# Optimization experiments

Hardware: AMD Instinct MI355X
Metric: run time of the kernel (lower is better)

Reference implementation:

```python
import jax, jax.numpy as jnp
import numpy as np

B, S, D, E, N = 2, 1024, 1024, 64, 16  # batch, seq, model_dim, embedding_dim, num_splats


def setup_inputs() -> dict:
    key = jax.random.key(0)
    ks = jax.random.split(key, 8)
    inv_sqrt_d = 1.0 / np.sqrt(D)
    return {
        "token_embeddings": jax.random.normal(ks[0], (B, S, D), jnp.float32),
        # position encoder Linear(D, E)
        "pos_W": jax.random.normal(ks[1], (D, E), jnp.float32) * inv_sqrt_d,
        "pos_b": jnp.zeros((E,), jnp.float32),
        "positional_bias": jax.random.normal(ks[2], (1024, E), jnp.float32) * 0.01,
        "splat_positions": jax.random.normal(ks[3], (N, E), jnp.float32) * 0.2,
        "splat_log_scales": jnp.zeros((N,), jnp.float32),
        # q/k/v Linear(D, D, bias=False)
        "q_W": jax.random.normal(ks[4], (D, D), jnp.float32) * inv_sqrt_d,
        "k_W": jax.random.normal(ks[5], (D, D), jnp.float32) * inv_sqrt_d,
        "v_W": jax.random.normal(ks[6], (D, D), jnp.float32) * inv_sqrt_d,
        "splat_gates": jnp.full((N,), 0.5, jnp.float32),
        "residual_weight": jnp.asarray(0.8, jnp.float32),
        "ln_w": jnp.ones((D,), jnp.float32),
        "ln_b": jnp.zeros((D,), jnp.float32),
    }


def reference(token_embeddings, pos_W, pos_b, positional_bias, splat_positions,
              splat_log_scales, q_W, k_W, v_W, splat_gates, residual_weight,
              ln_w, ln_b):
    b, s, d = token_embeddings.shape
    # token positions in splat embedding space: tanh(Linear(x)) + pos_bias[:S]
    positions = jnp.tanh(token_embeddings @ pos_W + pos_b) + positional_bias[:s][None]  # [B,S,E]
    # spatial influence per splat: Gaussian of distance, clamped scales, floor 0.01
    diff = positions[:, :, None, :] - splat_positions[None, None]  # [B,S,N,E]
    dist_sq = jnp.sum(diff * diff, axis=-1)                         # [B,S,N]
    scales = jnp.clip(jnp.exp(splat_log_scales), 0.3, 2.0)
    influence = jnp.maximum(jnp.exp(-0.5 * dist_sq / (scales * scales)), 0.01)  # [B,S,N]

    q = token_embeddings @ q_W
    k = token_embeddings @ k_W
    v = token_embeddings @ v_W

    w = jnp.transpose(influence, (2, 0, 1))      # [N,B,S]
    qw = q[None] * w[..., None]                  # [N,B,S,D]
    kw = k[None] * w[..., None]
    scores = jnp.einsum('nbid,nbjd->nbij', qw, kw) / jnp.sqrt(jnp.asarray(d, jnp.float32))
    causal = jnp.tril(jnp.ones((s, s), bool))
    scores = jnp.where(causal[None, None], scores, -1e9)
    attn = jax.nn.softmax(scores, axis=-1)       # [N,B,S,S]
    out = jnp.einsum('nbij,bjd->nbid', attn, v)  # [N,B,S,D]

    gates = jax.nn.sigmoid(splat_gates)[:, None, None, None]
    combined = jnp.mean(out * gates, axis=0)     # [B,S,D]

    rw = jax.nn.sigmoid(residual_weight)
    o = rw * token_embeddings + (1.0 - rw) * combined
    # LayerNorm (eps=1e-5)
    mu = jnp.mean(o, axis=-1, keepdims=True)
    var = jnp.mean((o - mu) ** 2, axis=-1, keepdims=True)
    return (o - mu) / jnp.sqrt(var + 1e-5) * ln_w + ln_b
```

## Files before the change

kernel.cpp:

```cpp
#include <hip/hip_runtime.h>
#include <hip/hip_bf16.h>
#include <hip/hip_fp16.h>

using bf16 = __hip_bfloat16;
typedef __attribute__((ext_vector_type(8))) short short8;
typedef __attribute__((ext_vector_type(4))) float f32x4;

static constexpr int Bb = 2, Ss = 1024, Dd = 1024, Ee = 64, Nn = 16;

struct Params {
    const float *X, *posW, *posB, *pbias, *spos, *lsc, *qW, *kW, *vW, *gates, *rwp, *lnw, *lnb;
    bf16 *Xb, *Wt, *WpT, *QKV, *Vt, *Aav;
    __half *wh;
    float *qk[4], *cb[4], *out;
};

__device__ __forceinline__ unsigned short f2bfr(float f) {
    __hip_bfloat16 h = __float2bfloat16(f);
    return *reinterpret_cast<unsigned short*>(&h);
}

#define GL_LDS(gp, lp) __builtin_amdgcn_global_load_lds( \
    (const __attribute__((address_space(1))) void*)(gp), \
    (__attribute__((address_space(3))) void*)(lp), 16, 0, 0)

__device__ __forceinline__ void do_transpose_f2b(
    const float* __restrict__ in, bf16* __restrict__ out,
    int R, int C, int bx, int by, char* sm)
{
    float (*tile)[65] = (float(*)[65])sm;
    int tx = threadIdx.x & 63, ty = threadIdx.x >> 6;
    int r0 = by * 64, c0 = bx * 64;
    #pragma unroll
    for (int i = 0; i < 16; ++i)
        tile[ty + i*4][tx] = in[(long)(r0 + ty + i*4)*C + c0 + tx];
    __syncthreads();
    #pragma unroll
    for (int i = 0; i < 16; ++i)
        out[(long)(c0 + ty + i*4)*R + r0 + tx] = __float2bfloat16(tile[tx][ty + i*4]);
    __syncthreads();
}

__device__ __forceinline__ void do_gemm64(
    const bf16* __restrict__ Ab, const bf16* __restrict__ Bw, float* __restrict__ C,
    int Nc, int m0, int n0, int kBeg, int kEnd, float scale, char* sm)
{
    int tid = threadIdx.x, wid = tid >> 6, lane = tid & 63;
    int wn = wid * 32, r16 = lane & 15, quad = lane >> 4;

    f32x4 acc[4][2];
    #pragma unroll
    for (int i = 0; i < 4; ++i)
        #pragma unroll
        for (int j = 0; j < 2; ++j)
            #pragma unroll
            for (int c = 0; c < 4; ++c) acc[i][j][c] = 0.f;

    const short* Ag = (const short*)Ab;
    const short* Bg = (const short*)Bw;

    int arow[2], akg[2], brow[4], bkg[4];
    #pragma unroll
    for (int j = 0; j < 2; ++j) {
        int c = tid + j*256; arow[j] = c >> 3; akg[j] = (c & 7) ^ (arow[j] & 7);
    }
    #pragma unroll
    for (int j = 0; j < 4; ++j) {
        int c = tid + j*256; brow[j] = c >> 3; bkg[j] = (c & 7) ^ (brow[j] & 7);
    }

    auto stage = [&](int k0, int cr) {
        short* sA = (short*)(sm + cr*24576);
        short* sB = (short*)(sm + cr*24576 + 8192);
        #pragma unroll
        for (int j = 0; j < 2; ++j)
            GL_LDS(Ag + (long)(m0 + arow[j])*1024 + k0 + akg[j]*8, sA + (tid + j*256)*8);
        #pragma unroll
        for (int j = 0; j < 4; ++j)
            GL_LDS(Bg + (long)(n0 + brow[j])*1024 + k0 + bkg[j]*8, sB + (tid + j*256)*8);
    };

    stage(kBeg, 0);
    __syncthreads();
    int cur = 0;
    for (int k0 = kBeg; k0 < kEnd; k0 += 64) {
        if (k0 + 64 < kEnd) stage(k0 + 64, cur ^ 1);
        short* lA = (short*)(sm + cur*24576);
        short* lB = (short*)(sm + cur*24576 + 8192);
        #pragma unroll
        for (int kk = 0; kk < 2; ++kk) {
            int kc = kk*4 + quad;
            short8 af[4], bfv[2];
            #pragma unroll
            for (int i = 0; i < 4; ++i) {
                int r = i*16 + r16;
                af[i] = *(const short8*)(lA + r*64 + (kc ^ (r & 7))*8);
            }
            #pragma unroll
            for (int j = 0; j < 2; ++j) {
                int r = wn + j*16 + r16;
                bfv[j] = *(const short8*)(lB + r*64 + (kc ^ (r & 7))*8);
            }
            #pragma unroll
            for (int i = 0; i < 4; ++i)
                #pragma unroll
                for (int j = 0; j < 2; ++j)
                    acc[i][j] = __builtin_amdgcn_mfma_f32_16x16x32_bf16(af[i], bfv[j], acc[i][j], 0, 0, 0);
        }
        __syncthreads();
        cur ^= 1;
    }

    #pragma unroll
    for (int i = 0; i < 4; ++i)
        #pragma unroll
        for (int j = 0; j < 2; ++j)
            #pragma unroll
            for (int rr = 0; rr < 4; ++rr)
                C[(long)(m0 + i*16 + quad*4 + rr)*Nc + n0 + wn + j*16 + r16] =
                    acc[i][j][rr] * scale;
}

template<int OUT_MODE>
__device__ __forceinline__ void do_gemm128(
    const bf16* __restrict__ Ab, const bf16* __restrict__ Bw, void* __restrict__ Cv,
    int Nc, int m0, int n0, char* sm)
{
    int tid = threadIdx.x, wid = tid >> 6, lane = tid & 63;
    int wm = (wid >> 1) * 64, wnn = (wid & 1) * 64;
    int r16 = lane & 15, quad = lane >> 4;

    f32x4 acc[4][4];
    #pragma unroll
    for (int i = 0; i < 4; ++i)
        #pragma unroll
        for (int j = 0; j < 4; ++j)
            #pragma unroll
            for (int c = 0; c < 4; ++c) acc[i][j][c] = 0.f;

    const short* Ag = (const short*)Ab;
    const short* Bg = (const short*)Bw;

    int rowc[4], kgc[4];
    #pragma unroll
    for (int j = 0; j < 4; ++j) {
        int c = tid + j*256; rowc[j] = c >> 3; kgc[j] = (c & 7) ^ (rowc[j] & 7);
    }

    auto stage = [&](int k0, int cr) {
        short* sA = (short*)(sm + cr*32768);
        short* sB = (short*)(sm + cr*32768 + 16384);
        #pragma unroll
        for (int j = 0; j < 4; ++j)
            GL_LDS(Ag + (long)(m0 + rowc[j])*1024 + k0 + kgc[j]*8, sA + (tid + j*256)*8);
        #pragma unroll
        for (int j = 0; j < 4; ++j)
            GL_LDS(Bg + (long)(n0 + rowc[j])*1024 + k0 + kgc[j]*8, sB + (tid + j*256)*8);
    };

    stage(0, 0);
    __syncthreads();
    int cur = 0;
    for (int k0 = 0; k0 < 1024; k0 += 64) {
        if (k0 + 64 < 1024) stage(k0 + 64, cur ^ 1);
        short* lA = (short*)(sm + cur*32768);
        short* lB = (short*)(sm + cur*32768 + 16384);
        #pragma unroll
        for (int kk = 0; kk < 2; ++kk) {
            int kc = kk*4 + quad;
            short8 af[4], bfv[4];
            #pragma unroll
            for (int i = 0; i < 4; ++i) {
                int r = wm + i*16 + r16;
                af[i] = *(const short8*)(lA + r*64 + (kc ^ (r & 7))*8);
            }
            #pragma unroll
            for (int j = 0; j < 4; ++j) {
                int r = wnn + j*16 + r16;
                bfv[j] = *(const short8*)(lB + r*64 + (kc ^ (r & 7))*8);
            }
            #pragma unroll
            for (int i = 0; i < 4; ++i)
                #pragma unroll
                for (int j = 0; j < 4; ++j)
                    acc[i][j] = __builtin_amdgcn_mfma_f32_16x16x32_bf16(af[i], bfv[j], acc[i][j], 0, 0, 0);
        }
        __syncthreads();
        cur ^= 1;
    }

    if (OUT_MODE == 1) {
        bf16* C = (bf16*)Cv;
        #pragma unroll
        for (int i = 0; i < 4; ++i)
            #pragma unroll
            for (int j = 0; j < 4; ++j)
                #pragma unroll
                for (int rr = 0; rr < 4; ++rr)
                    C[(long)(m0 + wm + i*16 + quad*4 + rr)*Nc + n0 + wnn + j*16 + r16] =
                        __float2bfloat16(acc[i][j][rr]);
    } else {
        __syncthreads();
        bf16 (*lt)[132] = (bf16(*)[132])sm;
        #pragma unroll
        for (int i = 0; i < 4; ++i)
            #pragma unroll
            for (int j = 0; j < 4; ++j)
                #pragma unroll
                for (int rr = 0; rr < 4; ++rr)
                    lt[wnn + j*16 + r16][wm + i*16 + quad*4 + rr] =
                        __float2bfloat16(acc[i][j][rr]);
        __syncthreads();
        bf16* Vb = (bf16*)Cv + (long)(m0 >> 10) * Dd * Ss;
        int s0 = m0 & (Ss - 1);
        int colBase = wid * 32 + (lane >> 4);
        int idx = (lane & 15) * 8;
        #pragma unroll
        for (int it = 0; it < 8; ++it) {
            int col = colBase + it * 4;
            ushort4 v0 = *(const ushort4*)&lt[col][idx];
            ushort4 v1 = *(const ushort4*)&lt[col][idx + 4];
            *(ushort4*)(Vb + (long)(n0 + col)*Ss + s0 + idx)     = v0;
            *(ushort4*)(Vb + (long)(n0 + col)*Ss + s0 + idx + 4) = v1;
        }
    }
}

__device__ __forceinline__ void do_pos(const Params& p, int m0, char* sm)
{
    float (*P)[65]  = (float(*)[65])(sm + 16384);
    float (*sp)[65] = (float(*)[65])(sm + 16384 + 64*65*4);

    int tid = threadIdx.x, wid = tid >> 6, lane = tid & 63;
    int r16 = lane & 15, quad = lane >> 4;

    for (int idx = tid; idx < 16*64; idx += 256)
        sp[idx >> 6][idx & 63] = p.spos[idx];

    f32x4 acc[4];
    #pragma unroll
    for (int j = 0; j < 4; ++j)
        #pragma unroll
        for (int c = 0; c < 4; ++c) acc[j][c] = 0.f;

    int ra = tid >> 2, ka = (tid & 3) * 8;
    const short* Ag = (const short*)p.Xb;
    const short* Bg = (const short*)p.WpT;

    auto stage = [&](int k0, int cr) {
        short* sA = (short*)(sm + cr*8192);
        short* sB = (short*)(sm + cr*8192 + 4096);
        GL_LDS(Ag + (long)(m0+ra)*1024 + k0 + ka, sA + tid*8);
        GL_LDS(Bg + (long)ra*1024 + k0 + ka,      sB + tid*8);
    };

    stage(0, 0);
    __syncthreads();
    int cur = 0;
    for (int k0 = 0; k0 < Dd; k0 += 32) {
        if (k0 + 32 < Dd) stage(k0 + 32, cur ^ 1);
        short* lA = (short*)(sm + cur*8192);
        short* lB = (short*)(sm + cur*8192 + 4096);
        short8 af = *(const short8*)(lA + (wid*16 + r16)*32 + quad*8);
        #pragma unroll
        for (int j = 0; j < 4; ++j) {
            short8 bfv = *(const short8*)(lB + (j*16 + r16)*32 + quad*8);
            acc[j] = __builtin_amdgcn_mfma_f32_16x16x32_bf16(af, bfv, acc[j], 0, 0, 0);
        }
        __syncthreads();
        cur ^= 1;
    }

    #pragma unroll
    for (int j = 0; j < 4; ++j)
        #pragma unroll
        for (int rr = 0; rr < 4; ++rr) {
            int rl  = wid*16 + quad*4 + rr;
            int col = j*16 + r16;
            int srow = (m0 + rl) & (Ss - 1);
            P[rl][col] = tanhf(acc[j][rr] + p.posB[col]) + p.pbias[srow*Ee + col];
        }
    __syncthreads();

    int n  = tid & 15;
    int rb = (tid >> 4) * 4;
    float sc = __expf(p.lsc[n]);
    sc = fminf(fmaxf(sc, 0.3f), 2.0f);
    float inv2 = -0.5f / (sc * sc);
    #pragma unroll
    for (int rr = 0; rr < 4; ++rr) {
        int row = rb + rr;
        float d2 = 0.f;
        #pragma unroll 16
        for (int e = 0; e < 64; ++e) {
            float df = P[row][e] - sp[n][e];
            d2 += df * df;
        }
        float infl = fmaxf(__expf(d2 * inv2), 0.01f);
        p.wh[(long)(m0 + row)*Nn + n] = __float2half(infl);
    }
}

__global__ __launch_bounds__(256) void k_prep(Params p)
{
    __shared__ __align__(16) char sm[64*65*4];
    int z = blockIdx.z;
    if (z < 3) {
        const float* w = (z == 0) ? p.qW : (z == 1) ? p.kW : p.vW;
        do_transpose_f2b(w, p.Wt + (long)z*Dd*Dd, Dd, Dd, blockIdx.x, blockIdx.y, sm);
    } else if (blockIdx.x == 0) {
        do_transpose_f2b(p.posW, p.WpT, Dd, Ee, 0, blockIdx.y, sm);
    } else {
        int job = blockIdx.y * 15 + (blockIdx.x - 1);
        const float4* src = (const float4*)p.X;
        ushort4* dst = (ushort4*)p.Xb;
        for (int idx = job*256 + (int)threadIdx.x; idx < Bb*Ss*Dd/4; idx += 240*256) {
            float4 v = src[idx];
            ushort4 y;
            y.x = f2bfr(v.x); y.y = f2bfr(v.y); y.z = f2bfr(v.z); y.w = f2bfr(v.w);
            dst[idx] = y;
        }
    }
}

__global__ __launch_bounds__(256) void k_qkv_pos(Params p)
{
    __shared__ __align__(16) char sm[65536];
    int job = blockIdx.x;
    if (job < 384) {
        int z = job >> 7, t = job & 127;
        int bm = t >> 3, bn = t & 7;
        if (z < 2)
            do_gemm128<1>(p.Xb, p.Wt + (long)z*Dd*Dd, p.QKV + (long)z*2048*1024,
                          Dd, bm*128, bn*128, sm);
        else
            do_gemm128<2>(p.Xb, p.Wt + (long)2*Dd*Dd, p.Vt,
                          Dd, bm*128, bn*128, sm);
    } else {
        do_pos(p, (job - 384)*64, sm);
    }
}

__global__ __launch_bounds__(256) void k_qkt(Params p)
{
    __shared__ __align__(16) char sm[49152];
    int job = blockIdx.x;
    int h = job & 3, pairIdx = job >> 2;
    int b = pairIdx / 72, t = pairIdx % 72;
    int acc = 0, bm = 0, bn = 0;
    #pragma unroll
    for (int u = 0; u < 16; ++u) {
        int c = (u >> 1) + 1;
        if (t < acc + c) { bm = u; bn = t - acc; break; }
        acc += c;
    }
    const bf16* Qb = p.QKV + (long)b*Ss*Dd;
    const bf16* Kb = p.QKV + (long)2048*1024 + (long)b*Ss*Dd;
    float* dst = p.qk[h] + (long)b*Ss*Ss;
    do_gemm64(Qb, Kb, dst, Ss, bm*64, bn*128, h*256, h*256 + 256, 0.03125f, sm);
}

__global__ __launch_bounds__(256) void k_softmax(Params p)
{
    __shared__ __align__(16) char sm[36864 + 256 + 16384];
    __half2 (*wt)[9] = (__half2(*)[9])sm;
    float (*wi4)[16] = (float(*)[16])(sm + 36864);
    float (*qc)[Ss]  = (float(*)[Ss])(sm + 36864 + 256);

    int base = blockIdx.x * 4, b = blockIdx.y;
    int tid = threadIdx.x, wid = tid >> 6, lane = tid & 63;
    int imax = base + 3;

    const __half*  whb  = p.wh + (long)b*Ss*Nn;
    const __half2* whb2 = (const __half2*)whb;

    for (int j = tid; j <= imax; j += 256) {
        #pragma unroll
        for (int h = 0; h < 8; ++h)
            wt[j][h] = whb2[j*8 + h];
    }
    if (tid < 64) wi4[tid >> 4][tid & 15] =
        __half2float(whb[(long)(base + (tid >> 4))*16 + (tid & 15)]);
    __syncthreads();

    int i = base + wid;
    long roff = ((long)b*Ss + i)*Ss;
    const float* q0 = p.qk[0] + roff;
    const float* q1 = p.qk[1] + roff;
    const float* q2 = p.qk[2] + roff;
    const float* q3 = p.qk[3] + roff;
    bf16* arow      = p.Aav + roff;

    float wiR[16], l[16];
    #pragma unroll
    for (int n = 0; n < 16; ++n) { wiR[n] = wi4[wid][n]; l[n] = 0.f; }

    for (int j = lane; j <= i; j += 64) {
        float q = (q0[j] + q1[j]) + (q2[j] + q3[j]);
        qc[wid][j] = q;
        #pragma unroll
        for (int h = 0; h < 8; ++h) {
            float2 f = __half22float2(wt[j][h]);
            l[2*h]     += __expf(wiR[2*h]     * f.x * q);
            l[2*h + 1] += __expf(wiR[2*h + 1] * f.y * q);
        }
    }
    #pragma unroll
    for (int n = 0; n < 16; ++n)
        #pragma unroll
        for (int off = 32; off > 0; off >>= 1)
            l[n] += __shfl_xor(l[n], off);

    float coef[16];
    #pragma unroll
    for (int n = 0; n < 16; ++n) {
        float g  = p.gates[n];
        float sg = 1.f / (1.f + __expf(-g));
        coef[n]  = sg / (16.f * l[n]);
    }

    int jLim = (i | 63) + 1;
    for (int j = lane; j < jLim; j += 64) {
        float a = 0.f;
        if (j <= i) {
            float q = qc[wid][j];
            #pragma unroll
            for (int h = 0; h < 8; ++h) {
                float2 f = __half22float2(wt[j][h]);
                a += coef[2*h]     * __expf(wiR[2*h]     * f.x * q);
                a += coef[2*h + 1] * __expf(wiR[2*h + 1] * f.y * q);
            }
        }
        arow[j] = __float2bfloat16(a);
    }
}

__global__ __launch_bounds__(256) void k_av(Params p)
{
    __shared__ __align__(16) char sm[49152];
    int job = blockIdx.x;
    int b  = job / 320;
    int r  = job % 320;
    int bn = r / 40;
    int u  = r % 40;
    int acc = 0, bm = 0, h = 0;
    #pragma unroll
    for (int m = 0; m < 16; ++m) {
        int c = (m >> 2) + 1;
        if (u < acc + c) { bm = m; h = u - acc; break; }
        acc += c;
    }
    int kBeg = h * 256;
    int kEnd = (bm + 1) * 64; if (kEnd > kBeg + 256) kEnd = kBeg + 256;

    const bf16* Ab = p.Aav + (long)b*Ss*Ss;
    const bf16* Bw = p.Vt + (long)b*Dd*Ss;
    float* dst = p.cb[h] + (long)b*Ss*Dd;
    do_gemm64(Ab, Bw, dst, Dd, bm*64, bn*128, kBeg, kEnd, 1.f, sm);
}

__global__ __launch_bounds__(256) void k_epilogue(Params p)
{
    __shared__ float rs[4], rq[4];
    long row = blockIdx.x;
    int tid = threadIdx.x, wid = tid >> 6, lane = tid & 63;
    float rw = 1.f / (1.f + __expf(-p.rwp[0]));

    int s = (int)(row & (Ss - 1));
    float4 c = ((const float4*)(p.cb[0] + row*Dd))[tid];
    #pragma unroll
    for (int h = 1; h < 4; ++h) {
        if (s >= h*256) {
            float4 ch = ((const float4*)(p.cb[h] + row*Dd))[tid];
            c.x += ch.x; c.y += ch.y; c.z += ch.z; c.w += ch.w;
        }
    }
    float4 xv = ((const float4*)(p.X + row*Dd))[tid];

    float o[4];
    o[0] = rw * xv.x + (1.f - rw) * c.x;
    o[1] = rw * xv.y + (1.f - rw) * c.y;
    o[2] = rw * xv.z + (1.f - rw) * c.z;
    o[3] = rw * xv.w + (1.f - rw) * c.w;

    float sm1 = o[0] + o[1] + o[2] + o[3];
    float sq  = o[0]*o[0] + o[1]*o[1] + o[2]*o[2] + o[3]*o[3];
    #pragma unroll
    for (int off = 32; off > 0; off >>= 1) { sm1 += __shfl_xor(sm1, off); sq += __shfl_xor(sq, off); }
    if (lane == 0) { rs[wid] = sm1; rq[wid] = sq; }
    __syncthreads();
    sm1 = rs[0] + rs[1] + rs[2] + rs[3];
    sq  = rq[0] + rq[1] + rq[2] + rq[3];
    float mu  = sm1 * (1.f/1024.f);
    float var = sq * (1.f/1024.f) - mu*mu;
    float inv = rsqrtf(var + 1e-5f);

    float4 lw = ((const float4*)p.lnw)[tid];
    float4 lb = ((const float4*)p.lnb)[tid];
    float4 y;
    y.x = (o[0] - mu)*inv*lw.x + lb.x;
    y.y = (o[1] - mu)*inv*lw.y + lb.y;
    y.z = (o[2] - mu)*inv*lw.z + lb.z;
    y.w = (o[3] - mu)*inv*lw.w + lb.w;
    ((float4*)(p.out + row*Dd))[tid] = y;
}

extern "C" void kernel_launch(void* const* d_in, const int* in_sizes, int n_in,
                              void* d_out, int out_size, void* d_ws, size_t ws_size,
                              hipStream_t stream)
{
    Params prm;
    prm.X     = (const float*)d_in[0];
    prm.posW  = (const float*)d_in[1];
    prm.posB  = (const float*)d_in[2];
    prm.pbias = (const float*)d_in[3];
    prm.spos  = (const float*)d_in[4];
    prm.lsc   = (const float*)d_in[5];
    prm.qW    = (const float*)d_in[6];
    prm.kW    = (const float*)d_in[7];
    prm.vW    = (const float*)d_in[8];
    prm.gates = (const float*)d_in[9];
    prm.rwp   = (const float*)d_in[10];
    prm.lnw   = (const float*)d_in[11];
    prm.lnb   = (const float*)d_in[12];

    char* ws = (char*)d_ws;
    size_t off = 0;
    prm.Xb  = (bf16*)(ws + off);   off += (size_t)Bb*Ss*Dd*2;
    prm.Wt  = (bf16*)(ws + off);   off += (size_t)3*Dd*Dd*2;
    prm.WpT = (bf16*)(ws + off);   off += (size_t)Ee*Dd*2;
    prm.QKV = (bf16*)(ws + off);   off += (size_t)2*2048*1024*2;
    prm.Vt  = (bf16*)(ws + off);   off += (size_t)Bb*Dd*Ss*2;
    prm.Aav = (bf16*)(ws + off);   off += (size_t)Bb*Ss*Ss*2;
    prm.wh  = (__half*)(ws + off); off += (size_t)Bb*Ss*Nn*2;
    for (int h = 0; h < 4; ++h) { prm.qk[h] = (float*)(ws + off); off += (size_t)Bb*Ss*Ss*4; }
    for (int h = 0; h < 4; ++h) { prm.cb[h] = (float*)(ws + off); off += (size_t)Bb*Ss*Dd*4; }
    prm.out = (float*)d_out;
    (void)ws_size;

    k_prep    <<<dim3(16,16,4), 256, 0, stream>>>(prm);
    k_qkv_pos <<<416,            256, 0, stream>>>(prm);
    k_qkt     <<<576,            256, 0, stream>>>(prm);
    k_softmax <<<dim3(256, 2),   256, 0, stream>>>(prm);
    k_av      <<<640,            256, 0, stream>>>(prm);
    k_epilogue<<<2048,           256, 0, stream>>>(prm);
}
```

Measured before the change: 160.2 us.

## Replace split-K partial GEMMs with full-K 64x64 tiles in QK^T and AV

The QK^T and AV GEMMs previously split K into four 256-wide chunks written to separate fp32 partial buffers, which softmax and the epilogue then summed. They now use 64x64 output tiles that run the full K range, so a single output buffer replaces the four partials. This removes the extra partial-buffer writes and reads and lets blocks skip fully masked causal tiles at finer granularity. In exchange, each block loops over a longer K with a smaller tile, giving fewer blocks in QK^T and less MFMA reuse per LDS load, plus load imbalance from the causal K lengths.

```diff
diff --git a/kernel.cpp b/kernel.cpp
--- a/kernel.cpp
+++ b/kernel.cpp
@@ -12,7 +12,7 @@
     const float *X, *posW, *posB, *pbias, *spos, *lsc, *qW, *kW, *vW, *gates, *rwp, *lnw, *lnb;
     bf16 *Xb, *Wt, *WpT, *QKV, *Vt, *Aav;
     __half *wh;
-    float *qk[4], *cb[4], *out;
+    float *qk, *cb, *out;
 };
 
 __device__ __forceinline__ unsigned short f2bfr(float f) {
@@ -41,43 +41,36 @@
     __syncthreads();
 }
 
-__device__ __forceinline__ void do_gemm64(
+__device__ __forceinline__ void do_gemm6464(
     const bf16* __restrict__ Ab, const bf16* __restrict__ Bw, float* __restrict__ C,
     int Nc, int m0, int n0, int kBeg, int kEnd, float scale, char* sm)
 {
     int tid = threadIdx.x, wid = tid >> 6, lane = tid & 63;
-    int wn = wid * 32, r16 = lane & 15, quad = lane >> 4;
-
-    f32x4 acc[4][2];
-    #pragma unroll
-    for (int i = 0; i < 4; ++i)
-        #pragma unroll
-        for (int j = 0; j < 2; ++j)
-            #pragma unroll
-            for (int c = 0; c < 4; ++c) acc[i][j][c] = 0.f;
+    int r16 = lane & 15, quad = lane >> 4;
+
+    f32x4 acc[4];
+    #pragma unroll
+    for (int j = 0; j < 4; ++j)
+        #pragma unroll
+        for (int c = 0; c < 4; ++c) acc[j][c] = 0.f;
 
     const short* Ag = (const short*)Ab;
     const short* Bg = (const short*)Bw;
 
-    int arow[2], akg[2], brow[4], bkg[4];
+    int row2[2], kg2[2];
     #pragma unroll
     for (int j = 0; j < 2; ++j) {
-        int c = tid + j*256; arow[j] = c >> 3; akg[j] = (c & 7) ^ (arow[j] & 7);
-    }
-    #pragma unroll
-    for (int j = 0; j < 4; ++j) {
-        int c = tid + j*256; brow[j] = c >> 3; bkg[j] = (c & 7) ^ (brow[j] & 7);
+        int c = tid + j*256; row2[j] = c >> 3; kg2[j] = (c & 7) ^ (row2[j] & 7);
     }
 
     auto stage = [&](int k0, int cr) {
-        short* sA = (short*)(sm + cr*24576);
-        short* sB = (short*)(sm + cr*24576 + 8192);
-        #pragma unroll
-        for (int j = 0; j < 2; ++j)
-            GL_LDS(Ag + (long)(m0 + arow[j])*1024 + k0 + akg[j]*8, sA + (tid + j*256)*8);
-        #pragma unroll
-        for (int j = 0; j < 4; ++j)
-            GL_LDS(Bg + (long)(n0 + brow[j])*1024 + k0 + bkg[j]*8, sB + (tid + j*256)*8);
+        short* sA = (short*)(sm + cr*16384);
+        short* sB = (short*)(sm + cr*16384 + 8192);
+        #pragma unroll
+        for (int j = 0; j < 2; ++j) {
+            GL_LDS(Ag + (long)(m0 + row2[j])*1024 + k0 + kg2[j]*8, sA + (tid + j*256)*8);
+            GL_LDS(Bg + (long)(n0 + row2[j])*1024 + k0 + kg2[j]*8, sB + (tid + j*256)*8);
+        }
     };
 
     stage(kBeg, 0);
@@ -85,40 +78,30 @@
     int cur = 0;
     for (int k0 = kBeg; k0 < kEnd; k0 += 64) {
         if (k0 + 64 < kEnd) stage(k0 + 64, cur ^ 1);
-        short* lA = (short*)(sm + cur*24576);
-        short* lB = (short*)(sm + cur*24576 + 8192);
+        short* lA = (short*)(sm + cur*16384);
+        short* lB = (short*)(sm + cur*16384 + 8192);
         #pragma unroll
         for (int kk = 0; kk < 2; ++kk) {
             int kc = kk*4 + quad;
-            short8 af[4], bfv[2];
-            #pragma unroll
-            for (int i = 0; i < 4; ++i) {
-                int r = i*16 + r16;
-                af[i] = *(const short8*)(lA + r*64 + (kc ^ (r & 7))*8);
+            int ra = wid*16 + r16;
+            short8 af = *(const short8*)(lA + ra*64 + (kc ^ (ra & 7))*8);
+            #pragma unroll
+            for (int j = 0; j < 4; ++j) {
+                int rb = j*16 + r16;
+                short8 bfv = *(const short8*)(lB + rb*64 + (kc ^ (rb & 7))*8);
+                acc[j] = __builtin_amdgcn_mfma_f32_16x16x32_bf16(af, bfv, acc[j], 0, 0, 0);
             }
-            #pragma unroll
-            for (int j = 0; j < 2; ++j) {
-                int r = wn + j*16 + r16;
-                bfv[j] = *(const short8*)(lB + r*64 + (kc ^ (r & 7))*8);
-            }
-            #pragma unroll
-            for (int i = 0; i < 4; ++i)
-                #pragma unroll
-                for (int j = 0; j < 2; ++j)
-                    acc[i][j] = __builtin_amdgcn_mfma_f32_16x16x32_bf16(af[i], bfv[j], acc[i][j], 0, 0, 0);
         }
         __syncthreads();
         cur ^= 1;
     }
 
     #pragma unroll
-    for (int i = 0; i < 4; ++i)
-        #pragma unroll
-        for (int j = 0; j < 2; ++j)
-            #pragma unroll
-            for (int rr = 0; rr < 4; ++rr)
-                C[(long)(m0 + i*16 + quad*4 + rr)*Nc + n0 + wn + j*16 + r16] =
-                    acc[i][j][rr] * scale;
+    for (int j = 0; j < 4; ++j)
+        #pragma unroll
+        for (int rr = 0; rr < 4; ++rr)
+            C[(long)(m0 + wid*16 + quad*4 + rr)*Nc + n0 + j*16 + r16] =
+                acc[j][rr] * scale;
 }
 
 template<int OUT_MODE>
@@ -343,21 +326,20 @@
 
 __global__ __launch_bounds__(256) void k_qkt(Params p)
 {
-    __shared__ __align__(16) char sm[49152];
+    __shared__ __align__(16) char sm[32768];
     int job = blockIdx.x;
-    int h = job & 3, pairIdx = job >> 2;
-    int b = pairIdx / 72, t = pairIdx % 72;
+    int b = job / 136, t = job % 136;
     int acc = 0, bm = 0, bn = 0;
     #pragma unroll
     for (int u = 0; u < 16; ++u) {
-        int c = (u >> 1) + 1;
+        int c = u + 1;
         if (t < acc + c) { bm = u; bn = t - acc; break; }
         acc += c;
     }
     const bf16* Qb = p.QKV + (long)b*Ss*Dd;
     const bf16* Kb = p.QKV + (long)2048*1024 + (long)b*Ss*Dd;
-    float* dst = p.qk[h] + (long)b*Ss*Ss;
-    do_gemm64(Qb, Kb, dst, Ss, bm*64, bn*128, h*256, h*256 + 256, 0.03125f, sm);
+    float* dst = p.qk + (long)b*Ss*Ss;
+    do_gemm6464(Qb, Kb, dst, Ss, bm*64, bn*64, 0, 1024, 0.03125f, sm);
 }
 
 __global__ __launch_bounds__(256) void k_softmax(Params p)
@@ -385,10 +367,7 @@
 
     int i = base + wid;
     long roff = ((long)b*Ss + i)*Ss;
-    const float* q0 = p.qk[0] + roff;
-    const float* q1 = p.qk[1] + roff;
-    const float* q2 = p.qk[2] + roff;
-    const float* q3 = p.qk[3] + roff;
+    const float* q0 = p.qk + roff;
     bf16* arow      = p.Aav + roff;
 
     float wiR[16], l[16];
@@ -396,7 +375,7 @@
     for (int n = 0; n < 16; ++n) { wiR[n] = wi4[wid][n]; l[n] = 0.f; }
 
     for (int j = lane; j <= i; j += 64) {
-        float q = (q0[j] + q1[j]) + (q2[j] + q3[j]);
+        float q = q0[j];
         qc[wid][j] = q;
         #pragma unroll
         for (int h = 0; h < 8; ++h) {
@@ -437,26 +416,18 @@
 
 __global__ __launch_bounds__(256) void k_av(Params p)
 {
-    __shared__ __align__(16) char sm[49152];
+    __shared__ __align__(16) char sm[32768];
     int job = blockIdx.x;
-    int b  = job / 320;
-    int r  = job % 320;
-    int bn = r / 40;
-    int u  = r % 40;
-    int acc = 0, bm = 0, h = 0;
-    #pragma unroll
-    for (int m = 0; m < 16; ++m) {
-        int c = (m >> 2) + 1;
-        if (u < acc + c) { bm = m; h = u - acc; break; }
-        acc += c;
-    }
-    int kBeg = h * 256;
-    int kEnd = (bm + 1) * 64; if (kEnd > kBeg + 256) kEnd = kBeg + 256;
+    int b  = job >> 8;
+    int r  = job & 255;
+    int bm = 15 - (r >> 4);
+    int bn = r & 15;
+    int kEnd = (bm + 1) * 64;
 
     const bf16* Ab = p.Aav + (long)b*Ss*Ss;
     const bf16* Bw = p.Vt + (long)b*Dd*Ss;
-    float* dst = p.cb[h] + (long)b*Ss*Dd;
-    do_gemm64(Ab, Bw, dst, Dd, bm*64, bn*128, kBeg, kEnd, 1.f, sm);
+    float* dst = p.cb + (long)b*Ss*Dd;
+    do_gemm6464(Ab, Bw, dst, Dd, bm*64, bn*64, 0, kEnd, 1.f, sm);
 }
 
 __global__ __launch_bounds__(256) void k_epilogue(Params p)
@@ -466,15 +437,7 @@
     int tid = threadIdx.x, wid = tid >> 6, lane = tid & 63;
     float rw = 1.f / (1.f + __expf(-p.rwp[0]));
 
-    int s = (int)(row & (Ss - 1));
-    float4 c = ((const float4*)(p.cb[0] + row*Dd))[tid];
-    #pragma unroll
-    for (int h = 1; h < 4; ++h) {
-        if (s >= h*256) {
-            float4 ch = ((const float4*)(p.cb[h] + row*Dd))[tid];
-            c.x += ch.x; c.y += ch.y; c.z += ch.z; c.w += ch.w;
-        }
-    }
+    float4 c  = ((const float4*)(p.cb + row*Dd))[tid];
     float4 xv = ((const float4*)(p.X + row*Dd))[tid];
 
     float o[4];
@@ -533,15 +496,15 @@
     prm.Vt  = (bf16*)(ws + off);   off += (size_t)Bb*Dd*Ss*2;
     prm.Aav = (bf16*)(ws + off);   off += (size_t)Bb*Ss*Ss*2;
     prm.wh  = (__half*)(ws + off); off += (size_t)Bb*Ss*Nn*2;
-    for (int h = 0; h < 4; ++h) { prm.qk[h] = (float*)(ws + off); off += (size_t)Bb*Ss*Ss*4; }
-    for (int h = 0; h < 4; ++h) { prm.cb[h] = (float*)(ws + off); off += (size_t)Bb*Ss*Dd*4; }
+    prm.qk  = (float*)(ws + off);  off += (size_t)Bb*Ss*Ss*4;
+    prm.cb  = (float*)(ws + off);  off += (size_t)Bb*Ss*Dd*4;
     prm.out = (float*)d_out;
     (void)ws_size;
 
     k_prep    <<<dim3(16,16,4), 256, 0, stream>>>(prm);
     k_qkv_pos <<<416,            256, 0, stream>>>(prm);
-    k_qkt     <<<576,            256, 0, stream>>>(prm);
+    k_qkt     <<<272,            256, 0, stream>>>(prm);
     k_softmax <<<dim3(256, 2),   256, 0, stream>>>(prm);
-    k_av      <<<640,            256, 0, stream>>>(prm);
+    k_av      <<<512,            256, 0, stream>>>(prm);
     k_epilogue<<<2048,           256, 0, stream>>>(prm);
 }
```

Result: slower. 165.2 us (+3.1%).
